# Kernel optimization log

Hardware: AMD Instinct MI355X
Metric: run time of the kernel (lower is better)

## Reference

```python
import jax, jax.numpy as jnp
from jax import lax
import numpy as np

NHEADS = 8

def _conv_block2d(x, w, b):
    y = lax.conv_general_dilated(x, w, (2, 2), [(1, 1), (1, 1)],
                                 dimension_numbers=('NCHW', 'OIHW', 'NCHW'))
    return jax.nn.gelu(y + b[None, :, None, None])

def _conv_block3d(x, w, b):
    y = lax.conv_general_dilated(x, w, (2, 2, 2), [(1, 1)] * 3,
                                 dimension_numbers=('NCDHW', 'OIDHW', 'NCDHW'))
    return jax.nn.gelu(y + b[None, :, None, None, None])

def _layernorm(x, g, b, eps=1e-5):
    mu = x.mean(-1, keepdims=True)
    var = x.var(-1, keepdims=True)
    return (x - mu) / jnp.sqrt(var + eps) * g + b

def _neighborhood_attn(x, g, bln, qkv_w, qkv_b, proj_w, proj_b, dw=5, hw=7, ww=7):
    # x: [B, C, D, H, W]; 3D neighborhood attention, window (dw,hw,ww), zero-pad + mask
    B, C, D, H, W = x.shape
    h, hd = NHEADS, C // NHEADS
    xt = jnp.transpose(x, (0, 2, 3, 4, 1))               # [B,D,H,W,C]
    y = _layernorm(xt, g, bln)
    qkv = y @ qkv_w + qkv_b                               # [B,D,H,W,3C]
    qkv = qkv.reshape(B, D, H, W, 3, h, hd)
    qkv = jnp.transpose(qkv, (4, 0, 5, 6, 1, 2, 3))       # [3,B,h,hd,D,H,W]
    q, k, v = qkv[0] * (hd ** -0.5), qkv[1], qkv[2]
    pz, py, px = dw // 2, hw // 2, ww // 2
    pad = ((0, 0), (0, 0), (0, 0), (pz, pz), (py, py), (px, px))
    kp, vp = jnp.pad(k, pad), jnp.pad(v, pad)
    valid = jnp.pad(jnp.ones((D, H, W), x.dtype), ((pz, pz), (py, py), (px, px)))
    offs = jnp.stack(jnp.meshgrid(jnp.arange(dw), jnp.arange(hw), jnp.arange(ww), indexing='ij'), -1).reshape(-1, 3)

    def score_step(_, o):
        ks = lax.dynamic_slice(kp, (0, 0, 0, o[0], o[1], o[2]), (B, h, hd, D, H, W))
        m = lax.dynamic_slice(valid, (o[0], o[1], o[2]), (D, H, W))
        return None, ((q * ks).sum(2), m)

    _, (scores, masks) = lax.scan(score_step, None, offs)  # [245,B,h,D,H,W],[245,D,H,W]
    neg = jnp.finfo(scores.dtype).min
    scores = jnp.where(masks[:, None, None] > 0, scores, neg)
    probs = jax.nn.softmax(scores, axis=0)

    def out_step(acc, xs):
        o, p = xs
        vs = lax.dynamic_slice(vp, (0, 0, 0, o[0], o[1], o[2]), (B, h, hd, D, H, W))
        return acc + p[:, :, None] * vs, None

    out0 = jnp.zeros((B, h, hd, D, H, W), x.dtype)
    out, _ = lax.scan(out_step, out0, (offs, probs))
    out = jnp.transpose(out, (0, 3, 4, 5, 1, 2)).reshape(B, D, H, W, C)
    out = out @ proj_w + proj_b
    return x + jnp.transpose(out, (0, 4, 1, 2, 3))

def setup_inputs() -> dict:
    key = jax.random.key(0)
    ks = jax.random.split(key, 16)
    rn = lambda i, shp, s: jax.random.normal(ks[i], shp, jnp.float32) * s
    return {
        'x_2d': rn(0, (1, 8, 256, 512), 1.0),
        'x_3d': rn(1, (1, 5, 24, 256, 512), 1.0),
        'sw0': rn(2, (128, 8, 3, 3), 0.02), 'sb0': jnp.zeros((128,), jnp.float32),
        'sw1': rn(3, (256, 128, 3, 3), 0.02), 'sb1': jnp.zeros((256,), jnp.float32),
        'sw2': rn(4, (512, 256, 3, 3), 0.02), 'sb2': jnp.zeros((512,), jnp.float32),
        'pw0': rn(5, (128, 5, 3, 3, 3), 0.02), 'pb0': jnp.zeros((128,), jnp.float32),
        'pw1': rn(6, (256, 128, 3, 3, 3), 0.02), 'pb1': jnp.zeros((256,), jnp.float32),
        'pw2': rn(7, (512, 256, 3, 3, 3), 0.02), 'pb2': jnp.zeros((512,), jnp.float32),
        'lat_w': rn(8, (512, 512, 1, 1, 1), 0.02), 'lat_b': jnp.zeros((512,), jnp.float32),
        'ln_g': jnp.ones((3, 512), jnp.float32), 'ln_b': jnp.zeros((3, 512), jnp.float32),
        'qkv_w': rn(9, (3, 512, 1536), 0.02), 'qkv_b': jnp.zeros((3, 1536), jnp.float32),
        'proj_w': rn(10, (3, 512, 512), 0.02), 'proj_b': jnp.zeros((3, 512), jnp.float32),
    }

def reference(x_2d, x_3d, sw0, sb0, sw1, sb1, sw2, sb2,
              pw0, pb0, pw1, pb1, pw2, pb2, lat_w, lat_b,
              ln_g, ln_b, qkv_w, qkv_b, proj_w, proj_b):
    s = x_2d
    for w_, b_ in ((sw0, sb0), (sw1, sb1), (sw2, sb2)):
        s = _conv_block2d(s, w_, b_)
    p = x_3d
    for w_, b_ in ((pw0, pb0), (pw1, pb1), (pw2, pb2)):
        p = _conv_block3d(p, w_, b_)
    feats = jnp.concatenate([p, s[:, :, None]], axis=2)   # [B,512,D/8+1,H/8,W/8]
    lat = lax.conv_general_dilated(feats, lat_w, (1, 1, 1), 'VALID',
                                   dimension_numbers=('NCDHW', 'OIDHW', 'NCDHW'))
    lat = lat + lat_b[None, :, None, None, None]
    for i in range(3):
        lat = _neighborhood_attn(lat, ln_g[i], ln_b[i], qkv_w[i], qkv_b[i], proj_w[i], proj_b[i])
    return lat
```

## Files before the change

### kernel.cpp

```cpp
#include <hip/hip_runtime.h>
#include <hip/hip_bf16.h>
#include <math.h>

typedef __hip_bfloat16 bf16;
typedef __attribute__((ext_vector_type(8))) short s8v;
typedef __attribute__((ext_vector_type(4))) float f4v;

__device__ __forceinline__ float ldf(const float* p) { return *p; }
__device__ __forceinline__ float ldf(const bf16* p) { return __bfloat162float(*p); }
__device__ __forceinline__ void stf(float* p, float v) { *p = v; }
__device__ __forceinline__ void stf(bf16* p, float v) { *p = __float2bfloat16(v); }

__device__ __forceinline__ float gelu_tanh(float x) {
    float x3 = x * x * x;
    return 0.5f * x * (1.f + tanhf(0.7978845608028654f * (x + 0.044715f * x3)));
}
__device__ __forceinline__ unsigned short bfbits(float x) {
    bf16 t = __float2bfloat16(x);
    return *(unsigned short*)&t;
}

__device__ __forceinline__ void gload16(const bf16* g, bf16* l)
{
    __builtin_amdgcn_global_load_lds(
        (const __attribute__((address_space(1))) unsigned int*)g,
        (__attribute__((address_space(3))) unsigned int*)l,
        16, 0, 0);
}

__global__ __launch_bounds__(256) void fill0_k(uint4* __restrict__ p, int n16)
{
    int i = blockIdx.x * 256 + threadIdx.x;
    if (i < n16) p[i] = uint4{0u, 0u, 0u, 0u};
}

__global__ __launch_bounds__(256) void wprep_k(const float* __restrict__ w, bf16* __restrict__ wr,
                                               int OC, int IC, int T)
{
    int i = blockIdx.x * 256 + threadIdx.x;
    if (i >= OC * IC * T) return;
    int t = i % T; int rem = i / T; int ic = rem % IC; int oc = rem / IC;
    wr[((size_t)t * OC + oc) * IC + ic] = __float2bfloat16(w[i]);
}

__global__ __launch_bounds__(256) void w1prep_k(const float* __restrict__ w, bf16* __restrict__ o,
                                                int OC, int nic, int ntap, int Kp)
{
    int i = blockIdx.x * 256 + threadIdx.x;
    if (i >= OC * Kp) return;
    int oc = i / Kp, k = i - oc * Kp;
    float v = 0.f;
    if (k < nic * ntap) {
        int tap = k / nic, ic = k - tap * nic;
        v = w[((size_t)oc * nic + ic) * ntap + tap];
    }
    o[i] = __float2bfloat16(v);
}

__global__ __launch_bounds__(256) void tprep_k(const float* __restrict__ w, bf16* __restrict__ wt,
                                               int K, int N)
{
    int i = blockIdx.x * 256 + threadIdx.x;
    if (i >= K * N) return;
    int n = i % N, k = i / N;
    wt[(size_t)n * K + k] = __float2bfloat16(w[i]);
}

__global__ __launch_bounds__(256) void cast_k(const float* __restrict__ w, bf16* __restrict__ o, int n)
{
    int i = blockIdx.x * 256 + threadIdx.x;
    if (i < n) o[i] = __float2bfloat16(w[i]);
}

__global__ __launch_bounds__(256) void im2col3d_k(const float* __restrict__ x, bf16* __restrict__ A, int od0)
{
    int gid = blockIdx.x * 256 + threadIdx.x;
    int m = gid / 20, kg = gid - 20 * (gid / 20);
    int ow = m & 255, rowid = m >> 8;
    int oh = rowid & 127, od = od0 + (rowid >> 7);
    int iz0 = 2 * od - 1, iy0 = 2 * oh - 1, ix0 = 2 * ow - 1;
    union { uint4 u; unsigned short h[8]; } pk;
#pragma unroll
    for (int j = 0; j < 8; j++) {
        int k = kg * 8 + j;
        float v = 0.f;
        if (k < 135) {
            int tap = k / 5, ic = k - tap * 5;
            int kz = tap / 9, r = tap - kz * 9;
            int ky = r / 3, kx = r - ky * 3;
            int iz = iz0 + kz, iy = iy0 + ky, ix = ix0 + kx;
            if ((unsigned)iz < 24u && (unsigned)iy < 256u && (unsigned)ix < 512u)
                v = x[(((size_t)ic * 24 + iz) * 256 + iy) * 512 + ix];
        }
        pk.h[j] = bfbits(v);
    }
    *(uint4*)&A[(size_t)m * 160 + kg * 8] = pk.u;
}

__global__ __launch_bounds__(256) void im2col2d_k(const float* __restrict__ x, bf16* __restrict__ A)
{
    int gid = blockIdx.x * 256 + threadIdx.x;
    int m = gid / 12, kg = gid - 12 * (gid / 12);
    int ow = m & 255, oh = m >> 8;
    int iy0 = 2 * oh - 1, ix0 = 2 * ow - 1;
    union { uint4 u; unsigned short h[8]; } pk;
#pragma unroll
    for (int j = 0; j < 8; j++) {
        int k = kg * 8 + j;
        float v = 0.f;
        if (k < 72) {
            int tap = k >> 3, ic = k & 7;
            int ky = tap / 3, kx = tap - ky * 3;
            int iy = iy0 + ky, ix = ix0 + kx;
            if ((unsigned)iy < 256u && (unsigned)ix < 512u)
                v = x[((size_t)ic * 256 + iy) * 512 + ix];
        }
        pk.h[j] = bfbits(v);
    }
    *(uint4*)&A[(size_t)m * 96 + kg * 8] = pk.u;
}

__global__ __launch_bounds__(256) void conv1_gemm(
    const bf16* __restrict__ A, const bf16* __restrict__ W, const float* __restrict__ bias,
    bf16* __restrict__ out, int M, int Kp, int rowOff)
{
    __shared__ __align__(16) bf16 As[128 * 32];
    __shared__ __align__(16) bf16 Bs[128 * 32];
    int tid = threadIdx.x;
    int m0 = blockIdx.x * 128;
    int wave = tid >> 6, lane = tid & 63;
    int wb = tid & 192;
    int wm = (wave >> 1) * 64, wn = (wave & 1) * 64;
    int lm = lane & 15, lq = lane >> 4;
    f4v acc[4][4];
#pragma unroll
    for (int i = 0; i < 4; i++)
#pragma unroll
        for (int j = 0; j < 4; j++) acc[i][j] = f4v{0.f, 0.f, 0.f, 0.f};
    for (int k0 = 0; k0 < Kp; k0 += 32) {
        __syncthreads();
#pragma unroll
        for (int c = 0; c < 2; c++) {
            int i = c * 256 + tid;
            int row = i >> 2, kq = i & 3;
            gload16(&A[(size_t)(m0 + row) * Kp + k0 + kq * 8], &As[(c * 256 + wb) * 8]);
            gload16(&W[(size_t)row * Kp + k0 + kq * 8], &Bs[(c * 256 + wb) * 8]);
        }
        __syncthreads();
        s8v af[4], bfr[4];
#pragma unroll
        for (int mi = 0; mi < 4; mi++) af[mi] = *(const s8v*)&As[(wm + mi * 16 + lm) * 32 + lq * 8];
#pragma unroll
        for (int ni = 0; ni < 4; ni++) bfr[ni] = *(const s8v*)&Bs[(wn + ni * 16 + lm) * 32 + lq * 8];
#pragma unroll
        for (int mi = 0; mi < 4; mi++)
#pragma unroll
            for (int ni = 0; ni < 4; ni++)
                acc[mi][ni] = __builtin_amdgcn_mfma_f32_16x16x32_bf16(af[mi], bfr[ni], acc[mi][ni], 0, 0, 0);
    }
#pragma unroll
    for (int mi = 0; mi < 4; mi++)
#pragma unroll
        for (int ni = 0; ni < 4; ni++)
#pragma unroll
            for (int r = 0; r < 4; r++) {
                int m = m0 + wm + mi * 16 + lq * 4 + r;
                int n = wn + ni * 16 + lm;
                int row = rowOff + (m >> 8), x = m & 255;
                float v = acc[mi][ni][r] + bias[n];
                out[((size_t)row * 258 + 1 + x) * 128 + n] = __float2bfloat16(gelu_tanh(v));
            }
}

template <int BM, int KD>
__global__ __launch_bounds__(256) void conv_mfma2(
    const bf16* __restrict__ in, const bf16* __restrict__ wr, const float* __restrict__ bias,
    bf16* __restrict__ out, int ID, int IH, int IWp, int IC,
    int OH, int OC, int OWS, int outPad, int nx)
{
    constexpr int NI = (BM == 128) ? 4 : 2;
    __shared__ __align__(16) bf16 As[3 * BM * 32];
    __shared__ __align__(16) bf16 Bs[3 * 128 * 32];
    int tid = threadIdx.x;
    int nwg = gridDim.x;
    int bl = blockIdx.x;
    int swz = (bl & 7) * (nwg >> 3) + (bl >> 3);
    int n0 = (swz % nx) * 128;
    int rowid = swz / nx;
    int od = rowid / OH, oh = rowid % OH;
    int wave = tid >> 6, lane = tid & 63;
    int wb = tid & 192;
    int wm = (BM == 128) ? (wave >> 1) * 64 : 0;
    int wn = (BM == 128) ? (wave & 1) * 64 : wave * 32;
    int lm = lane & 15, lq = lane >> 4;
    f4v acc[4][NI];
#pragma unroll
    for (int i = 0; i < 4; i++)
#pragma unroll
        for (int j = 0; j < NI; j++) acc[i][j] = f4v{0.f, 0.f, 0.f, 0.f};

    for (int kz = 0; kz < KD; kz++) {
        int iz = (KD == 3) ? (2 * od + kz - 1) : 0;
        if ((unsigned)iz >= (unsigned)ID) continue;
        for (int ky = 0; ky < 3; ky++) {
            int iy = 2 * oh + ky - 1;
            if ((unsigned)iy >= (unsigned)IH) continue;
            const bf16* inrow = in + ((size_t)iz * IH + iy) * IWp * IC;
            const bf16* wbase = wr + (size_t)((kz * 3 + ky) * 3) * OC * IC;
            for (int kb = 0; kb < IC; kb += 32) {
                __syncthreads();
#pragma unroll
                for (int c = 0; c < (3 * BM) / 64; c++) {
                    int i = c * 256 + tid;
                    int kx = i / (BM * 4);
                    int r = i - kx * (BM * 4);
                    int m = r >> 2, sub = r & 3;
                    gload16(&inrow[(size_t)(2 * m + kx) * IC + kb + sub * 8],
                            &As[(c * 256 + wb) * 8]);
                }
#pragma unroll
                for (int c = 0; c < 6; c++) {
                    int i = c * 256 + tid;
                    int t3 = i >> 9, r = i & 511, n = r >> 2, sub = r & 3;
                    gload16(&wbase[((size_t)t3 * OC + n0 + n) * IC + kb + sub * 8],
                            &Bs[(c * 256 + wb) * 8]);
                }
                __syncthreads();
#pragma unroll
                for (int kx = 0; kx < 3; kx++) {
                    s8v af[4], bfr[NI];
#pragma unroll
                    for (int mi = 0; mi < 4; mi++)
                        af[mi] = *(const s8v*)&As[(kx * BM + wm + mi * 16 + lm) * 32 + lq * 8];
#pragma unroll
                    for (int ni = 0; ni < NI; ni++)
                        bfr[ni] = *(const s8v*)&Bs[(kx * 128 + wn + ni * 16 + lm) * 32 + lq * 8];
#pragma unroll
                    for (int mi = 0; mi < 4; mi++)
#pragma unroll
                        for (int ni = 0; ni < NI; ni++)
                            acc[mi][ni] = __builtin_amdgcn_mfma_f32_16x16x32_bf16(af[mi], bfr[ni], acc[mi][ni], 0, 0, 0);
                }
            }
        }
    }
    size_t orowbase = ((size_t)rowid * OWS + outPad) * OC;
#pragma unroll
    for (int mi = 0; mi < 4; mi++)
#pragma unroll
        for (int ni = 0; ni < NI; ni++)
#pragma unroll
            for (int r = 0; r < 4; r++) {
                int m = wm + mi * 16 + lq * 4 + r;
                int n = n0 + wn + ni * 16 + lm;
                float v = acc[mi][ni][r] + bias[n];
                out[orowbase + (size_t)m * OC + n] = __float2bfloat16(gelu_tanh(v));
            }
}

template <typename OutT, int RES, int VT>
__global__ __launch_bounds__(256) void gemm_bt(
    const bf16* __restrict__ A, const bf16* __restrict__ Bt, const float* __restrict__ bias,
    OutT* __restrict__ C, const float* __restrict__ res, bf16* __restrict__ vt,
    int M, int N, int K)
{
    __shared__ __align__(16) bf16 As[128 * 32];
    __shared__ __align__(16) bf16 Bs[128 * 32];
    int tid = threadIdx.x;
    int n0 = blockIdx.x * 128, m0 = blockIdx.y * 128;
    int wave = tid >> 6, lane = tid & 63;
    int wb = tid & 192;
    int wm = (wave >> 1) * 64, wn = (wave & 1) * 64;
    int lm = lane & 15, lq = lane >> 4;
    f4v acc[4][4];
#pragma unroll
    for (int i = 0; i < 4; i++)
#pragma unroll
        for (int j = 0; j < 4; j++) acc[i][j] = f4v{0.f, 0.f, 0.f, 0.f};
    for (int k0 = 0; k0 < K; k0 += 32) {
        __syncthreads();
#pragma unroll
        for (int c = 0; c < 2; c++) {
            int i = c * 256 + tid;
            int row = i >> 2, kq = i & 3;
            gload16(&A[(size_t)(m0 + row) * K + k0 + kq * 8], &As[(c * 256 + wb) * 8]);
            gload16(&Bt[(size_t)(n0 + row) * K + k0 + kq * 8], &Bs[(c * 256 + wb) * 8]);
        }
        __syncthreads();
        s8v af[4], bfr[4];
#pragma unroll
        for (int mi = 0; mi < 4; mi++) af[mi] = *(const s8v*)&As[(wm + mi * 16 + lm) * 32 + lq * 8];
#pragma unroll
        for (int ni = 0; ni < 4; ni++) bfr[ni] = *(const s8v*)&Bs[(wn + ni * 16 + lm) * 32 + lq * 8];
#pragma unroll
        for (int mi = 0; mi < 4; mi++)
#pragma unroll
            for (int ni = 0; ni < 4; ni++)
                acc[mi][ni] = __builtin_amdgcn_mfma_f32_16x16x32_bf16(af[mi], bfr[ni], acc[mi][ni], 0, 0, 0);
    }
#pragma unroll
    for (int mi = 0; mi < 4; mi++)
#pragma unroll
        for (int ni = 0; ni < 4; ni++) {
            int n = n0 + wn + ni * 16 + lm;
            int mbase = m0 + wm + mi * 16 + lq * 4;
            float b = bias[n];
            if (VT && n >= 1024) {
                ushort4 pk;
                pk.x = bfbits(acc[mi][ni][0] + b);
                pk.y = bfbits(acc[mi][ni][1] + b);
                pk.z = bfbits(acc[mi][ni][2] + b);
                pk.w = bfbits(acc[mi][ni][3] + b);
                *(ushort4*)&vt[(size_t)(n - 1024) * 8192 + mbase] = pk;
            }
#pragma unroll
            for (int r = 0; r < 4; r++) {
                int m = mbase + r;
                float v = acc[mi][ni][r] + b;
                if (RES) v += res[(size_t)m * N + n];
                stf(&C[(size_t)m * N + n], v);
            }
        }
}

__global__ __launch_bounds__(256) void ln_k(
    const float* __restrict__ lat, const float* __restrict__ g, const float* __restrict__ b,
    bf16* __restrict__ y)
{
    int tok = blockIdx.x * 4 + (threadIdx.x >> 6);
    int lane = threadIdx.x & 63;
    const float4* row = (const float4*)&lat[(size_t)tok * 512 + lane * 8];
    float4 a = row[0], c = row[1];
    float s = a.x + a.y + a.z + a.w + c.x + c.y + c.z + c.w;
    float ss = a.x * a.x + a.y * a.y + a.z * a.z + a.w * a.w
             + c.x * c.x + c.y * c.y + c.z * c.z + c.w * c.w;
#pragma unroll
    for (int off = 32; off; off >>= 1) {
        s += __shfl_xor(s, off);
        ss += __shfl_xor(ss, off);
    }
    float mu = s * (1.f / 512.f);
    float var = ss * (1.f / 512.f) - mu * mu;
    float rstd = rsqrtf(var + 1e-5f);
    const float4* gp = (const float4*)&g[lane * 8];
    const float4* bp = (const float4*)&b[lane * 8];
    float4 g0 = gp[0], g1 = gp[1], b0 = bp[0], b1 = bp[1];
    union { uint4 u; unsigned short h[8]; } pk;
    pk.h[0] = bfbits((a.x - mu) * rstd * g0.x + b0.x);
    pk.h[1] = bfbits((a.y - mu) * rstd * g0.y + b0.y);
    pk.h[2] = bfbits((a.z - mu) * rstd * g0.z + b0.z);
    pk.h[3] = bfbits((a.w - mu) * rstd * g0.w + b0.w);
    pk.h[4] = bfbits((c.x - mu) * rstd * g1.x + b1.x);
    pk.h[5] = bfbits((c.y - mu) * rstd * g1.y + b1.y);
    pk.h[6] = bfbits((c.z - mu) * rstd * g1.z + b1.z);
    pk.h[7] = bfbits((c.w - mu) * rstd * g1.w + b1.w);
    *(uint4*)&y[(size_t)tok * 512 + lane * 8] = pk.u;
}

__global__ __launch_bounds__(256) void natt_mfma(
    const bf16* __restrict__ qkv, const bf16* __restrict__ vT, bf16* __restrict__ o)
{
    __shared__ __align__(16) char smem[53248];
    bf16* qs = (bf16*)smem;
    float* obuf = (float*)smem;
    float* mlb = (float*)(smem + 51200);
    int tid = threadIdx.x;
    int rowid = blockIdx.x;
    int head = blockIdx.y;
    int d = rowid >> 5, h = rowid & 31;
    int rowbase = rowid * 64;
    int hoff = head * 64;
    int wave = tid >> 6, lane = tid & 63;
    int lm = lane & 15, lq = lane >> 4;
    bf16* pb = (bf16*)(smem + 10240 + wave * 10240);

    for (int i = tid; i < 512; i += 256) {
        int row = i >> 3, sub = i & 7;
        *(uint4*)&qs[row * 80 + sub * 8] =
            *(const uint4*)&qkv[(size_t)(rowbase + row) * 1536 + hoff + sub * 8];
    }
    __syncthreads();
    s8v qf[4][2];
#pragma unroll
    for (int mi = 0; mi < 4; mi++)
#pragma unroll
        for (int c = 0; c < 2; c++)
            qf[mi][c] = *(const s8v*)&qs[(mi * 16 + lm) * 80 + c * 32 + lq * 8];

    f4v Oa[4][4];
#pragma unroll
    for (int i = 0; i < 4; i++)
#pragma unroll
        for (int j = 0; j < 4; j++) Oa[i][j] = f4v{0.f, 0.f, 0.f, 0.f};
    float mr[4][4], lr[4][4];
#pragma unroll
    for (int i = 0; i < 4; i++)
#pragma unroll
        for (int j = 0; j < 4; j++) { mr[i][j] = -1e30f; lr[i][j] = 0.f; }

    for (int idx = wave; idx < 35; idx += 4) {
        int dz = idx / 7 - 2, dy = idx % 7 - 3;
        int zz = d + dz, yy = h + dy;
        if ((unsigned)zz >= 4u || (unsigned)yy >= 32u) continue;
        int kbase = (zz * 32 + yy) * 64;
        f4v s[4][4];
#pragma unroll
        for (int i = 0; i < 4; i++)
#pragma unroll
            for (int j = 0; j < 4; j++) s[i][j] = f4v{0.f, 0.f, 0.f, 0.f};
        {
            s8v kf[4][2];
#pragma unroll
            for (int ni = 0; ni < 4; ni++)
#pragma unroll
                for (int c = 0; c < 2; c++)
                    kf[ni][c] = *(const s8v*)&qkv[(size_t)(kbase + ni * 16 + lm) * 1536 + 512 + hoff + c * 32 + lq * 8];
#pragma unroll
            for (int c = 0; c < 2; c++)
#pragma unroll
                for (int mi = 0; mi < 4; mi++)
#pragma unroll
                    for (int ni = 0; ni < 4; ni++)
                        s[mi][ni] = __builtin_amdgcn_mfma_f32_16x16x32_bf16(qf[mi][c], kf[ni][c], s[mi][ni], 0, 0, 0);
        }
#pragma unroll
        for (int mi = 0; mi < 4; mi++) {
#pragma unroll
            for (int r = 0; r < 4; r++) {
                int w0 = mi * 16 + lq * 4 + r;
                float sv[4];
                float rm = -1e30f;
#pragma unroll
                for (int ni = 0; ni < 4; ni++) {
                    int xp = ni * 16 + lm;
                    float v = s[mi][ni][r] * 0.125f;
                    v = ((unsigned)(xp - w0 + 3) <= 6u) ? v : -1e30f;
                    sv[ni] = v;
                    rm = fmaxf(rm, v);
                }
#pragma unroll
                for (int off = 1; off <= 8; off <<= 1)
                    rm = fmaxf(rm, __shfl_xor(rm, off));
                float mn = fmaxf(mr[mi][r], rm);
                float al = __expf(mr[mi][r] - mn);
                mr[mi][r] = mn;
                float rs = 0.f;
#pragma unroll
                for (int ni = 0; ni < 4; ni++) {
                    float p = __expf(sv[ni] - mn);
                    rs += p;
                    pb[w0 * 80 + ni * 16 + lm] = __float2bfloat16(p);
                }
#pragma unroll
                for (int off = 1; off <= 8; off <<= 1)
                    rs += __shfl_xor(rs, off);
                lr[mi][r] = lr[mi][r] * al + rs;
#pragma unroll
                for (int nd = 0; nd < 4; nd++)
                    Oa[mi][nd][r] *= al;
            }
        }
        __asm__ __volatile__("s_waitcnt lgkmcnt(0)" ::: "memory");
        {
            s8v pf[4][2], vf[4][2];
#pragma unroll
            for (int mi = 0; mi < 4; mi++)
#pragma unroll
                for (int c = 0; c < 2; c++)
                    pf[mi][c] = *(const s8v*)&pb[(mi * 16 + lm) * 80 + c * 32 + lq * 8];
#pragma unroll
            for (int nd = 0; nd < 4; nd++)
#pragma unroll
                for (int c = 0; c < 2; c++)
                    vf[nd][c] = *(const s8v*)&vT[(size_t)(hoff + nd * 16 + lm) * 8192 + kbase + c * 32 + lq * 8];
#pragma unroll
            for (int c = 0; c < 2; c++)
#pragma unroll
                for (int mi = 0; mi < 4; mi++)
#pragma unroll
                    for (int nd = 0; nd < 4; nd++)
                        Oa[mi][nd] = __builtin_amdgcn_mfma_f32_16x16x32_bf16(pf[mi][c], vf[nd][c], Oa[mi][nd], 0, 0, 0);
        }
    }
    if (lm == 0) {
#pragma unroll
        for (int mi = 0; mi < 4; mi++)
#pragma unroll
            for (int r = 0; r < 4; r++) {
                int row = mi * 16 + lq * 4 + r;
                mlb[wave * 128 + row] = mr[mi][r];
                mlb[wave * 128 + 64 + row] = lr[mi][r];
            }
    }
    __syncthreads();
    for (int wv = 0; wv < 4; wv++) {
        if (wave == wv) {
#pragma unroll
            for (int mi = 0; mi < 4; mi++)
#pragma unroll
                for (int r = 0; r < 4; r++) {
                    int row = mi * 16 + lq * 4 + r;
                    float M = fmaxf(fmaxf(mlb[row], mlb[128 + row]),
                                    fmaxf(mlb[256 + row], mlb[384 + row]));
                    float sc = __expf(mr[mi][r] - M);
#pragma unroll
                    for (int nd = 0; nd < 4; nd++) {
                        int ci = row * 65 + nd * 16 + lm;
                        float add = Oa[mi][nd][r] * sc;
                        obuf[ci] = (wv == 0) ? add : (obuf[ci] + add);
                    }
                }
        }
        __syncthreads();
    }
    {
        int row = tid >> 2, cb = (tid & 3) * 16;
        float m0 = mlb[row], m1 = mlb[128 + row], m2 = mlb[256 + row], m3 = mlb[384 + row];
        float M = fmaxf(fmaxf(m0, m1), fmaxf(m2, m3));
        float L = mlb[64 + row] * __expf(m0 - M) + mlb[192 + row] * __expf(m1 - M)
                + mlb[320 + row] * __expf(m2 - M) + mlb[448 + row] * __expf(m3 - M);
        float inv = 1.f / L;
        union { uint4 u[2]; unsigned short hs[16]; } pk;
#pragma unroll
        for (int j = 0; j < 16; j++)
            pk.hs[j] = bfbits(obuf[row * 65 + cb + j] * inv);
        *(uint4*)&o[(size_t)(rowbase + row) * 512 + hoff + cb] = pk.u[0];
        *(uint4*)&o[(size_t)(rowbase + row) * 512 + hoff + cb + 8] = pk.u[1];
    }
}

__global__ __launch_bounds__(256) void tout_k(const float* __restrict__ lat, float* __restrict__ out)
{
    __shared__ float t[64][65];
    int p0 = blockIdx.x * 64, c0 = blockIdx.y * 64;
    for (int i = threadIdx.x; i < 4096; i += 256) {
        int r = i >> 6, cc = i & 63;
        t[r][cc] = lat[(size_t)(p0 + r) * 512 + c0 + cc];
    }
    __syncthreads();
    for (int i = threadIdx.x; i < 4096; i += 256) {
        int cc = i >> 6, r = i & 63;
        out[(size_t)(c0 + cc) * 8192 + p0 + r] = t[r][cc];
    }
}

extern "C" void kernel_launch(void* const* d_in, const int* in_sizes, int n_in,
                              void* d_out, int out_size, void* d_ws, size_t ws_size,
                              hipStream_t stream)
{
    const float* x2d = (const float*)d_in[0];
    const float* x3d = (const float*)d_in[1];
    const float* sw0 = (const float*)d_in[2];
    const float* sb0 = (const float*)d_in[3];
    const float* sw1 = (const float*)d_in[4];
    const float* sb1 = (const float*)d_in[5];
    const float* sw2 = (const float*)d_in[6];
    const float* sb2 = (const float*)d_in[7];
    const float* pw0 = (const float*)d_in[8];
    const float* pb0 = (const float*)d_in[9];
    const float* pw1 = (const float*)d_in[10];
    const float* pb1 = (const float*)d_in[11];
    const float* pw2 = (const float*)d_in[12];
    const float* pb2 = (const float*)d_in[13];
    const float* latw = (const float*)d_in[14];
    const float* latb = (const float*)d_in[15];
    const float* lng = (const float*)d_in[16];
    const float* lnb = (const float*)d_in[17];
    const float* qkvw = (const float*)d_in[18];
    const float* qkvb = (const float*)d_in[19];
    const float* projw = (const float*)d_in[20];
    const float* projb = (const float*)d_in[21];
    float* outp = (float*)d_out;

    char* ws = (char*)d_ws;
    bf16* p0pad = (bf16*)(ws + 0);
    bf16* wr3d2 = (bf16*)(ws + 101449728ull);
    bf16* wr3d3 = (bf16*)(ws + 103219200ull);
    bf16* wr2d2 = (bf16*)(ws + 110297088ull);
    bf16* wr2d3 = (bf16*)(ws + 110886912ull);
    bf16* qkvt  = (bf16*)(ws + 113246208ull);
    bf16* projt = (bf16*)(ws + 117964800ull);
    bf16* latbf = (bf16*)(ws + 119537664ull);
    bf16* w13d  = (bf16*)(ws + 120061952ull);
    bf16* w12d  = (bf16*)(ws + 120102912ull);
    bf16* p1pad = (bf16*)(ws + 120127488ull);
    bf16* s0pad = (bf16*)(ws + 145686528ull);
    bf16* s1pad = (bf16*)(ws + 154140672ull);
    bf16* featsT= (bf16*)(ws + 158400512ull);
    float* lat  = (float*)(ws + 166789120ull);
    bf16* A3 = (bf16*)(ws + 120127488ull);
    bf16* A2 = (bf16*)(ws + 158400512ull);
    bf16* ybf    = (bf16*)(ws + 0);
    bf16* qkvbuf = (bf16*)(ws + 8388608ull);
    bf16* attno  = (bf16*)(ws + 33554432ull);
    bf16* vT     = (bf16*)(ws + 41943040ull);

    wprep_k<<<3456, 256, 0, stream>>>(pw1, wr3d2, 256, 128, 27);
    wprep_k<<<13824, 256, 0, stream>>>(pw2, wr3d3, 512, 256, 27);
    wprep_k<<<1152, 256, 0, stream>>>(sw1, wr2d2, 256, 128, 9);
    wprep_k<<<4608, 256, 0, stream>>>(sw2, wr2d3, 512, 256, 9);
    for (int r = 0; r < 3; r++) {
        tprep_k<<<3072, 256, 0, stream>>>(qkvw + (size_t)r * 786432, qkvt + (size_t)r * 786432, 512, 1536);
        tprep_k<<<1024, 256, 0, stream>>>(projw + (size_t)r * 262144, projt + (size_t)r * 262144, 512, 512);
    }
    cast_k<<<1024, 256, 0, stream>>>(latw, latbf, 262144);
    w1prep_k<<<80, 256, 0, stream>>>(pw0, w13d, 128, 5, 27, 160);
    w1prep_k<<<48, 256, 0, stream>>>(sw0, w12d, 128, 8, 9, 96);

    fill0_k<<<24768, 256, 0, stream>>>((uint4*)p0pad, 6340608);

    im2col3d_k<<<15360, 256, 0, stream>>>(x3d, A3, 0);
    conv1_gemm<<<1536, 256, 0, stream>>>(A3, w13d, pb0, p0pad, 196608, 160, 0);
    im2col3d_k<<<15360, 256, 0, stream>>>(x3d, A3, 6);
    conv1_gemm<<<1536, 256, 0, stream>>>(A3, w13d, pb0, p0pad, 196608, 160, 768);

    fill0_k<<<9344, 256, 0, stream>>>((uint4*)p1pad, 2392064);
    im2col2d_k<<<1536, 256, 0, stream>>>(x2d, A2);
    conv1_gemm<<<256, 256, 0, stream>>>(A2, w12d, sb0, s0pad, 32768, 96, 0);

    conv_mfma2<128, 1><<<dim3(128), 256, 0, stream>>>(s0pad, wr2d2, sb1, s1pad, 1, 128, 258, 128, 64, 256, 130, 1, 2);
    conv_mfma2<64, 1><<<dim3(128), 256, 0, stream>>>(s1pad, wr2d3, sb2, featsT + (size_t)6144 * 512, 1, 64, 130, 256, 32, 512, 64, 0, 4);
    conv_mfma2<128, 3><<<dim3(768), 256, 0, stream>>>(p0pad, wr3d2, pb1, p1pad, 12, 128, 258, 128, 64, 256, 130, 1, 2);
    conv_mfma2<64, 3><<<dim3(384), 256, 0, stream>>>(p1pad, wr3d3, pb2, featsT, 6, 64, 130, 256, 32, 512, 64, 0, 4);

    gemm_bt<float, 0, 0><<<dim3(4, 64), 256, 0, stream>>>(featsT, latbf, latb, lat, nullptr, nullptr, 8192, 512, 512);

    for (int r = 0; r < 3; r++) {
        ln_k<<<2048, 256, 0, stream>>>(lat, lng + r * 512, lnb + r * 512, ybf);
        gemm_bt<bf16, 0, 1><<<dim3(12, 64), 256, 0, stream>>>(ybf, qkvt + (size_t)r * 786432, qkvb + r * 1536,
                                                              qkvbuf, nullptr, vT, 8192, 1536, 512);
        natt_mfma<<<dim3(128, 8), 256, 0, stream>>>(qkvbuf, vT, attno);
        gemm_bt<float, 1, 0><<<dim3(4, 64), 256, 0, stream>>>(attno, projt + (size_t)r * 262144, projb + r * 512,
                                                              lat, lat, nullptr, 8192, 512, 512);
    }

    tout_k<<<dim3(128, 8), 256, 0, stream>>>(lat, outp);
}
```

Before: 1.499 ms.

## Software-pipeline K/V loads in neighborhood attention with swizzled P buffer

Restructures the natt_mfma window loop so the K fragment for the next valid window is prefetched while the current window's softmax runs, and V is loaded at the start of each iteration. It computes scores one mi row at a time to cut register pressure. It also replaces the padded P buffer with an XOR-swizzled 64-wide layout that reuses the Q staging area, shrinking LDS, and adds setprio around the MFMA blocks. The extra sync and live prefetch registers may raise VGPR use.

```diff
diff --git a/kernel.cpp b/kernel.cpp
--- a/kernel.cpp
+++ b/kernel.cpp
@@ -360,10 +360,10 @@
 __global__ __launch_bounds__(256) void natt_mfma(
     const bf16* __restrict__ qkv, const bf16* __restrict__ vT, bf16* __restrict__ o)
 {
-    __shared__ __align__(16) char smem[53248];
+    __shared__ __align__(16) char smem[34816];
     bf16* qs = (bf16*)smem;
     float* obuf = (float*)smem;
-    float* mlb = (float*)(smem + 51200);
+    float* mlb = (float*)(smem + 32768);
     int tid = threadIdx.x;
     int rowid = blockIdx.x;
     int head = blockIdx.y;
@@ -372,7 +372,7 @@
     int hoff = head * 64;
     int wave = tid >> 6, lane = tid & 63;
     int lm = lane & 15, lq = lane >> 4;
-    bf16* pb = (bf16*)(smem + 10240 + wave * 10240);
+    bf16* pb = (bf16*)(smem + wave * 8192);
 
     for (int i = tid; i < 512; i += 256) {
         int row = i >> 3, sub = i & 7;
@@ -386,6 +386,7 @@
 #pragma unroll
         for (int c = 0; c < 2; c++)
             qf[mi][c] = *(const s8v*)&qs[(mi * 16 + lm) * 80 + c * 32 + lq * 8];
+    __syncthreads();
 
     f4v Oa[4][4];
 #pragma unroll
@@ -398,42 +399,59 @@
 #pragma unroll
         for (int j = 0; j < 4; j++) { mr[i][j] = -1e30f; lr[i][j] = 0.f; }
 
-    for (int idx = wave; idx < 35; idx += 4) {
+    int idx = wave, kb = -1;
+    while (idx < 35) {
         int dz = idx / 7 - 2, dy = idx % 7 - 3;
         int zz = d + dz, yy = h + dy;
-        if ((unsigned)zz >= 4u || (unsigned)yy >= 32u) continue;
-        int kbase = (zz * 32 + yy) * 64;
-        f4v s[4][4];
-#pragma unroll
-        for (int i = 0; i < 4; i++)
-#pragma unroll
-            for (int j = 0; j < 4; j++) s[i][j] = f4v{0.f, 0.f, 0.f, 0.f};
-        {
-            s8v kf[4][2];
-#pragma unroll
-            for (int ni = 0; ni < 4; ni++)
-#pragma unroll
-                for (int c = 0; c < 2; c++)
-                    kf[ni][c] = *(const s8v*)&qkv[(size_t)(kbase + ni * 16 + lm) * 1536 + 512 + hoff + c * 32 + lq * 8];
+        if ((unsigned)zz < 4u && (unsigned)yy < 32u) { kb = (zz * 32 + yy) * 64; break; }
+        idx += 4;
+    }
+    s8v kf[4][2];
+    if (idx < 35) {
+#pragma unroll
+        for (int ni = 0; ni < 4; ni++)
 #pragma unroll
             for (int c = 0; c < 2; c++)
-#pragma unroll
-                for (int mi = 0; mi < 4; mi++)
-#pragma unroll
-                    for (int ni = 0; ni < 4; ni++)
-                        s[mi][ni] = __builtin_amdgcn_mfma_f32_16x16x32_bf16(qf[mi][c], kf[ni][c], s[mi][ni], 0, 0, 0);
-        }
+                kf[ni][c] = *(const s8v*)&qkv[(size_t)(kb + ni * 16 + lm) * 1536 + 512 + hoff + c * 32 + lq * 8];
+    }
+
+    while (idx < 35) {
+        int nidx = idx + 4, nkb = -1;
+        while (nidx < 35) {
+            int dz = nidx / 7 - 2, dy = nidx % 7 - 3;
+            int zz = d + dz, yy = h + dy;
+            if ((unsigned)zz < 4u && (unsigned)yy < 32u) { nkb = (zz * 32 + yy) * 64; break; }
+            nidx += 4;
+        }
+        s8v vf[4][2];
+#pragma unroll
+        for (int nd = 0; nd < 4; nd++)
+#pragma unroll
+            for (int c = 0; c < 2; c++)
+                vf[nd][c] = *(const s8v*)&vT[(size_t)(hoff + nd * 16 + lm) * 8192 + kb + c * 32 + lq * 8];
+
 #pragma unroll
         for (int mi = 0; mi < 4; mi++) {
+            f4v s[4];
+#pragma unroll
+            for (int ni = 0; ni < 4; ni++) s[ni] = f4v{0.f, 0.f, 0.f, 0.f};
+            __builtin_amdgcn_s_setprio(1);
+#pragma unroll
+            for (int c = 0; c < 2; c++)
+#pragma unroll
+                for (int ni = 0; ni < 4; ni++)
+                    s[ni] = __builtin_amdgcn_mfma_f32_16x16x32_bf16(qf[mi][c], kf[ni][c], s[ni], 0, 0, 0);
+            __builtin_amdgcn_s_setprio(0);
 #pragma unroll
             for (int r = 0; r < 4; r++) {
                 int w0 = mi * 16 + lq * 4 + r;
+                int sw = (w0 & 7) << 3;
                 float sv[4];
                 float rm = -1e30f;
 #pragma unroll
                 for (int ni = 0; ni < 4; ni++) {
                     int xp = ni * 16 + lm;
-                    float v = s[mi][ni][r] * 0.125f;
+                    float v = s[ni][r] * 0.125f;
                     v = ((unsigned)(xp - w0 + 3) <= 6u) ? v : -1e30f;
                     sv[ni] = v;
                     rm = fmaxf(rm, v);
@@ -449,7 +467,7 @@
                 for (int ni = 0; ni < 4; ni++) {
                     float p = __expf(sv[ni] - mn);
                     rs += p;
-                    pb[w0 * 80 + ni * 16 + lm] = __float2bfloat16(p);
+                    pb[(w0 << 6) + ((ni * 16 + lm) ^ sw)] = __float2bfloat16(p);
                 }
 #pragma unroll
                 for (int off = 1; off <= 8; off <<= 1)
@@ -460,19 +478,23 @@
                     Oa[mi][nd][r] *= al;
             }
         }
+        if (nidx < 35) {
+#pragma unroll
+            for (int ni = 0; ni < 4; ni++)
+#pragma unroll
+                for (int c = 0; c < 2; c++)
+                    kf[ni][c] = *(const s8v*)&qkv[(size_t)(nkb + ni * 16 + lm) * 1536 + 512 + hoff + c * 32 + lq * 8];
+        }
         __asm__ __volatile__("s_waitcnt lgkmcnt(0)" ::: "memory");
+        __builtin_amdgcn_sched_barrier(0);
         {
-            s8v pf[4][2], vf[4][2];
+            s8v pf[4][2];
 #pragma unroll
             for (int mi = 0; mi < 4; mi++)
 #pragma unroll
                 for (int c = 0; c < 2; c++)
-                    pf[mi][c] = *(const s8v*)&pb[(mi * 16 + lm) * 80 + c * 32 + lq * 8];
-#pragma unroll
-            for (int nd = 0; nd < 4; nd++)
-#pragma unroll
-                for (int c = 0; c < 2; c++)
-                    vf[nd][c] = *(const s8v*)&vT[(size_t)(hoff + nd * 16 + lm) * 8192 + kbase + c * 32 + lq * 8];
+                    pf[mi][c] = *(const s8v*)&pb[((mi * 16 + lm) << 6) + ((c * 32 + lq * 8) ^ ((lm & 7) << 3))];
+            __builtin_amdgcn_s_setprio(1);
 #pragma unroll
             for (int c = 0; c < 2; c++)
 #pragma unroll
@@ -480,7 +502,9 @@
 #pragma unroll
                     for (int nd = 0; nd < 4; nd++)
                         Oa[mi][nd] = __builtin_amdgcn_mfma_f32_16x16x32_bf16(pf[mi][c], vf[nd][c], Oa[mi][nd], 0, 0, 0);
-        }
+            __builtin_amdgcn_s_setprio(0);
+        }
+        idx = nidx; kb = nkb;
     }
     if (lm == 0) {
 #pragma unroll
```

New measurement: 1.421 ms. -5.1%, faster.

## Shrink LDS and registers in neighborhood attention kernel, sparsify softmax window

Applied to the files above, without the earlier changes.

Cuts the attention kernel's LDS from 53KB to 34KB by reusing the Q staging area for the per-wave P buffers. It pre-zeroes each P buffer and writes only the one in-window column per lane, using an XOR swizzle, and it adds launch bounds targeting 3 blocks per CU. The QK^T scores are now computed one row tile at a time to reduce live registers. The online softmax rescale is skipped unless some row max increases. V loads are issued before the LDS wait, MFMA sections get raised s_setprio, and block indices are remapped so that boundary rows are scheduled last. The single-column selection assumes each window fits in one 16-column group per lane and relies on the zero-filled P buffer staying valid across iterations.

```diff
diff --git a/kernel.cpp b/kernel.cpp
--- a/kernel.cpp
+++ b/kernel.cpp
@@ -357,22 +357,26 @@
     *(uint4*)&y[(size_t)tok * 512 + lane * 8] = pk.u;
 }
 
-__global__ __launch_bounds__(256) void natt_mfma(
+__global__ __launch_bounds__(256, 3) void natt_mfma(
     const bf16* __restrict__ qkv, const bf16* __restrict__ vT, bf16* __restrict__ o)
 {
-    __shared__ __align__(16) char smem[53248];
+    __shared__ __align__(16) char smem[34816];
     bf16* qs = (bf16*)smem;
     float* obuf = (float*)smem;
-    float* mlb = (float*)(smem + 51200);
+    float* mlb = (float*)(smem + 32768);
     int tid = threadIdx.x;
-    int rowid = blockIdx.x;
+    int bx = blockIdx.x;
+    int rd = bx >> 5, rh = bx & 31;
+    int d = (rd == 0) ? 1 : (rd == 1) ? 2 : (rd == 2) ? 0 : 3;
+    int h = (rh < 26) ? (rh + 3) : (rh == 26) ? 2 : (rh == 27) ? 29
+          : (rh == 28) ? 1 : (rh == 29) ? 30 : (rh == 30) ? 0 : 31;
+    int rowid = d * 32 + h;
     int head = blockIdx.y;
-    int d = rowid >> 5, h = rowid & 31;
     int rowbase = rowid * 64;
     int hoff = head * 64;
     int wave = tid >> 6, lane = tid & 63;
     int lm = lane & 15, lq = lane >> 4;
-    bf16* pb = (bf16*)(smem + 10240 + wave * 10240);
+    bf16* pb = (bf16*)(smem + wave * 8192);
 
     for (int i = tid; i < 512; i += 256) {
         int row = i >> 3, sub = i & 7;
@@ -386,6 +390,13 @@
 #pragma unroll
         for (int c = 0; c < 2; c++)
             qf[mi][c] = *(const s8v*)&qs[(mi * 16 + lm) * 80 + c * 32 + lq * 8];
+    __syncthreads();
+
+    {
+        uint4 z{0u, 0u, 0u, 0u};
+#pragma unroll
+        for (int i = 0; i < 8; i++) ((uint4*)pb)[lane + i * 64] = z;
+    }
 
     f4v Oa[4][4];
 #pragma unroll
@@ -403,76 +414,77 @@
         int zz = d + dz, yy = h + dy;
         if ((unsigned)zz >= 4u || (unsigned)yy >= 32u) continue;
         int kbase = (zz * 32 + yy) * 64;
-        f4v s[4][4];
-#pragma unroll
-        for (int i = 0; i < 4; i++)
-#pragma unroll
-            for (int j = 0; j < 4; j++) s[i][j] = f4v{0.f, 0.f, 0.f, 0.f};
-        {
-            s8v kf[4][2];
-#pragma unroll
-            for (int ni = 0; ni < 4; ni++)
-#pragma unroll
-                for (int c = 0; c < 2; c++)
-                    kf[ni][c] = *(const s8v*)&qkv[(size_t)(kbase + ni * 16 + lm) * 1536 + 512 + hoff + c * 32 + lq * 8];
+        s8v kf[4][2];
+#pragma unroll
+        for (int ni = 0; ni < 4; ni++)
 #pragma unroll
             for (int c = 0; c < 2; c++)
-#pragma unroll
-                for (int mi = 0; mi < 4; mi++)
-#pragma unroll
-                    for (int ni = 0; ni < 4; ni++)
-                        s[mi][ni] = __builtin_amdgcn_mfma_f32_16x16x32_bf16(qf[mi][c], kf[ni][c], s[mi][ni], 0, 0, 0);
-        }
+                kf[ni][c] = *(const s8v*)&qkv[(size_t)(kbase + ni * 16 + lm) * 1536 + 512 + hoff + c * 32 + lq * 8];
 #pragma unroll
         for (int mi = 0; mi < 4; mi++) {
+            f4v s[4];
+#pragma unroll
+            for (int ni = 0; ni < 4; ni++) s[ni] = f4v{0.f, 0.f, 0.f, 0.f};
+            __builtin_amdgcn_s_setprio(1);
+#pragma unroll
+            for (int c = 0; c < 2; c++)
+#pragma unroll
+                for (int ni = 0; ni < 4; ni++)
+                    s[ni] = __builtin_amdgcn_mfma_f32_16x16x32_bf16(qf[mi][c], kf[ni][c], s[ni], 0, 0, 0);
+            __builtin_amdgcn_s_setprio(0);
 #pragma unroll
             for (int r = 0; r < 4; r++) {
                 int w0 = mi * 16 + lq * 4 + r;
-                float sv[4];
-                float rm = -1e30f;
-#pragma unroll
-                for (int ni = 0; ni < 4; ni++) {
-                    int xp = ni * 16 + lm;
-                    float v = s[mi][ni][r] * 0.125f;
-                    v = ((unsigned)(xp - w0 + 3) <= 6u) ? v : -1e30f;
-                    sv[ni] = v;
-                    rm = fmaxf(rm, v);
-                }
+                float s0v = s[0][r], s1v = s[1][r], s2v = s[2][r], s3v = s[3][r];
+                int t = w0 + 8 - lm;
+                int niq = (t < 0) ? 0 : (t >> 4);
+                niq = (niq > 3) ? 3 : niq;
+                float vlo = (niq & 1) ? s1v : s0v;
+                float vhi = (niq & 1) ? s3v : s2v;
+                float v = (niq & 2) ? vhi : vlo;
+                int col = (niq << 4) | lm;
+                int dlt = col - w0;
+                float vv = ((unsigned)(dlt + 3) <= 6u) ? v * 0.125f : -1e30f;
+                float rm = vv;
 #pragma unroll
                 for (int off = 1; off <= 8; off <<= 1)
                     rm = fmaxf(rm, __shfl_xor(rm, off));
-                float mn = fmaxf(mr[mi][r], rm);
-                float al = __expf(mr[mi][r] - mn);
-                mr[mi][r] = mn;
-                float rs = 0.f;
-#pragma unroll
-                for (int ni = 0; ni < 4; ni++) {
-                    float p = __expf(sv[ni] - mn);
-                    rs += p;
-                    pb[w0 * 80 + ni * 16 + lm] = __float2bfloat16(p);
+                float mo = mr[mi][r];
+                float mn = mo;
+                if (__any(rm > mo)) {
+                    mn = fmaxf(mo, rm);
+                    float al = __expf(mo - mn);
+                    mr[mi][r] = mn;
+                    lr[mi][r] *= al;
+#pragma unroll
+                    for (int nd = 0; nd < 4; nd++)
+                        Oa[mi][nd][r] *= al;
                 }
+                float p = __expf(vv - mn);
+                float rs = p;
 #pragma unroll
                 for (int off = 1; off <= 8; off <<= 1)
                     rs += __shfl_xor(rs, off);
-                lr[mi][r] = lr[mi][r] * al + rs;
-#pragma unroll
-                for (int nd = 0; nd < 4; nd++)
-                    Oa[mi][nd][r] *= al;
+                lr[mi][r] += rs;
+                pb[(w0 << 6) + (col ^ ((w0 & 7) << 3))] = __float2bfloat16(p);
             }
         }
+        s8v vf[4][2];
+#pragma unroll
+        for (int nd = 0; nd < 4; nd++)
+#pragma unroll
+            for (int c = 0; c < 2; c++)
+                vf[nd][c] = *(const s8v*)&vT[(size_t)(hoff + nd * 16 + lm) * 8192 + kbase + c * 32 + lq * 8];
         __asm__ __volatile__("s_waitcnt lgkmcnt(0)" ::: "memory");
+        __builtin_amdgcn_sched_barrier(0);
         {
-            s8v pf[4][2], vf[4][2];
+            s8v pf[4][2];
 #pragma unroll
             for (int mi = 0; mi < 4; mi++)
 #pragma unroll
                 for (int c = 0; c < 2; c++)
-                    pf[mi][c] = *(const s8v*)&pb[(mi * 16 + lm) * 80 + c * 32 + lq * 8];
-#pragma unroll
-            for (int nd = 0; nd < 4; nd++)
-#pragma unroll
-                for (int c = 0; c < 2; c++)
-                    vf[nd][c] = *(const s8v*)&vT[(size_t)(hoff + nd * 16 + lm) * 8192 + kbase + c * 32 + lq * 8];
+                    pf[mi][c] = *(const s8v*)&pb[((mi * 16 + lm) << 6) + ((c * 32 + lq * 8) ^ ((lm & 7) << 3))];
+            __builtin_amdgcn_s_setprio(1);
 #pragma unroll
             for (int c = 0; c < 2; c++)
 #pragma unroll
@@ -480,6 +492,7 @@
 #pragma unroll
                     for (int nd = 0; nd < 4; nd++)
                         Oa[mi][nd] = __builtin_amdgcn_mfma_f32_16x16x32_bf16(pf[mi][c], vf[nd][c], Oa[mi][nd], 0, 0, 0);
+            __builtin_amdgcn_s_setprio(0);
         }
     }
     if (lm == 0) {
```

Measured after the change: 1.535 ms. 1.02x slower.
